# Optimization experiments

Hardware: AMD Instinct MI355X
Metric: run time of the kernel (lower is better)

## Reference

```python
import jax, jax.numpy as jnp
import numpy as np

DIM = 2048
N_HEADS = 16
N_KV_HEADS = 4
HEAD_DIM = 128
SLIDING_WINDOW = 1024
ROPE_BASE = 10000.0


def _rotate_half(x):
    d = x.shape[-1] // 2
    return jnp.concatenate((-x[..., d:], x[..., :d]), axis=-1)


def _rope_cos_sin(T, dtype):
    inv_freq = 1.0 / (ROPE_BASE ** (jnp.arange(0, HEAD_DIM, 2, dtype=jnp.float32) / HEAD_DIM))
    t = jnp.arange(T, dtype=jnp.float32)
    freqs = jnp.outer(t, inv_freq)            # [T, HEAD_DIM//2]
    emb = jnp.concatenate((freqs, freqs), axis=-1)  # [T, HEAD_DIM]
    return jnp.cos(emb).astype(dtype), jnp.sin(emb).astype(dtype)


def setup_inputs() -> dict:
    key = jax.random.key(0)
    kx, kq, kk, kv, ko = jax.random.split(key, 5)
    s_in = 1.0 / np.sqrt(DIM)
    s_o = 1.0 / np.sqrt(N_HEADS * HEAD_DIM)
    return {
        "x": jax.random.normal(kx, (1, 4096, DIM), dtype=jnp.float32),
        "Wq": jax.random.normal(kq, (DIM, N_HEADS * HEAD_DIM), dtype=jnp.float32) * s_in,
        "Wk": jax.random.normal(kk, (DIM, N_KV_HEADS * HEAD_DIM), dtype=jnp.float32) * s_in,
        "Wv": jax.random.normal(kv, (DIM, N_KV_HEADS * HEAD_DIM), dtype=jnp.float32) * s_in,
        "Wo": jax.random.normal(ko, (N_HEADS * HEAD_DIM, DIM), dtype=jnp.float32) * s_o,
    }


def reference(x, Wq, Wk, Wv, Wo):
    B, T, C = x.shape
    # projections -> [B, H, T, D]
    q = (x @ Wq).reshape(B, T, N_HEADS, HEAD_DIM).transpose(0, 2, 1, 3)
    k = (x @ Wk).reshape(B, T, N_KV_HEADS, HEAD_DIM).transpose(0, 2, 1, 3)
    v = (x @ Wv).reshape(B, T, N_KV_HEADS, HEAD_DIM).transpose(0, 2, 1, 3)

    cos, sin = _rope_cos_sin(T, x.dtype)      # [T, D], broadcast over B, H
    q = q * cos + _rotate_half(q) * sin
    k = k * cos + _rotate_half(k) * sin

    # GQA: repeat kv heads (repeat_interleave over head axis)
    kv_rep = N_HEADS // N_KV_HEADS
    k = jnp.repeat(k, kv_rep, axis=1)
    v = jnp.repeat(v, kv_rep, axis=1)

    scale = 1.0 / np.sqrt(HEAD_DIM)
    att = jnp.einsum("bhqd,bhkd->bhqk", q, k) * scale  # [B, H, T, T]

    i = jnp.arange(T)[:, None]
    j = jnp.arange(T)[None, :]
    allowed = (j <= i) & ((i - j) < SLIDING_WINDOW)     # causal + sliding window
    att = jnp.where(allowed, att, -jnp.inf)
    att = jax.nn.softmax(att, axis=-1)

    y = jnp.einsum("bhqk,bhkd->bhqd", att, v)           # [B, H, T, D]
    y = y.transpose(0, 2, 1, 3).reshape(B, T, N_HEADS * HEAD_DIM)
    return y @ Wo
```

## Files before the change

kernel.cpp:

```cpp
#include <hip/hip_runtime.h>
#include <math.h>

typedef __bf16 bf16;
typedef __bf16 bf16x8 __attribute__((ext_vector_type(8)));
typedef __bf16 bf16x4 __attribute__((ext_vector_type(4)));
typedef float f32x4 __attribute__((ext_vector_type(4)));

__device__ __forceinline__ void ldg_lds16(const bf16* g, bf16* l) {
#if __has_builtin(__builtin_amdgcn_global_load_lds)
    __builtin_amdgcn_global_load_lds(
        (const __attribute__((address_space(1))) void*)g,
        (__attribute__((address_space(3))) void*)l, 16, 0, 0);
#else
    *(bf16x8*)l = *(const bf16x8*)g;
#endif
}

__global__ void cvt_x(const float* __restrict__ X, bf16* __restrict__ Xb, int total8)
{
    int idx = blockIdx.x * 256 + threadIdx.x;
    if (idx >= total8) return;
    const float* p = X + (size_t)idx * 8;
    f32x4 a = *reinterpret_cast<const f32x4*>(p);
    f32x4 b = *reinterpret_cast<const f32x4*>(p + 4);
    bf16x8 r;
    r[0] = (bf16)a[0]; r[1] = (bf16)a[1]; r[2] = (bf16)a[2]; r[3] = (bf16)a[3];
    r[4] = (bf16)b[0]; r[5] = (bf16)b[1]; r[6] = (bf16)b[2]; r[7] = (bf16)b[3];
    *reinterpret_cast<bf16x8*>(Xb + (size_t)idx * 8) = r;
}

__global__ void cvt_wt3(const float* __restrict__ Wq, const float* __restrict__ Wk,
                        const float* __restrict__ Wv, bf16* __restrict__ Wt)
{
    __shared__ float t[32][33];
    int bx = blockIdx.x;
    const float* W; int Ncols, nbase;
    if (bx < 64)      { W = Wq; Ncols = 2048; nbase = 0;    }
    else if (bx < 80) { W = Wk; Ncols = 512;  nbase = 2048; bx -= 64; }
    else              { W = Wv; Ncols = 512;  nbase = 2560; bx -= 80; }
    const int n0 = bx * 32, k0 = blockIdx.y * 32;
    const int x = threadIdx.x, y = threadIdx.y;
    #pragma unroll
    for (int i = 0; i < 4; ++i)
        t[y + 8 * i][x] = W[(size_t)(k0 + y + 8 * i) * Ncols + n0 + x];
    __syncthreads();
    #pragma unroll
    for (int i = 0; i < 4; ++i)
        Wt[(size_t)(nbase + n0 + y + 8 * i) * 2048 + k0 + x] = (bf16)t[x][y + 8 * i];
}

__global__ void cvt_wt(const float* __restrict__ W, bf16* __restrict__ Wt, int Ncols)
{
    __shared__ float t[32][33];
    const int n0 = blockIdx.x * 32, k0 = blockIdx.y * 32;
    const int x = threadIdx.x, y = threadIdx.y;
    #pragma unroll
    for (int i = 0; i < 4; ++i)
        t[y + 8 * i][x] = W[(size_t)(k0 + y + 8 * i) * Ncols + n0 + x];
    __syncthreads();
    #pragma unroll
    for (int i = 0; i < 4; ++i)
        Wt[(size_t)(n0 + y + 8 * i) * 2048 + k0 + x] = (bf16)t[x][y + 8 * i];
}

__global__ __launch_bounds__(512, 2) void gemm256_qkv(
    const bf16* __restrict__ A, const bf16* __restrict__ Bt,
    bf16* __restrict__ Qo, bf16* __restrict__ Ko, bf16* __restrict__ Vt,
    int K)
{
    __shared__ __align__(16) bf16 smem[2 * 28672];

    const int tid  = threadIdx.x;
    const int lane = tid & 63;
    const int wave = tid >> 6;
    const int quad = lane >> 4;
    const int l16  = lane & 15;
    const int wm   = wave >> 2;
    const int wn   = wave & 3;

    const int m0 = blockIdx.y * 256;
    const int n0 = blockIdx.x * 192;

    int offA[4], offB[3];
    #pragma unroll
    for (int p = 0; p < 4; ++p) {
        int u = p * 512 + tid;
        int row = u >> 3;
        int kc8 = (u & 7) ^ (row & 7);
        offA[p] = (m0 + row) * K + kc8 * 8;
    }
    #pragma unroll
    for (int p = 0; p < 3; ++p) {
        int u = p * 512 + tid;
        int row = u >> 3;
        int kc8 = (u & 7) ^ (row & 7);
        offB[p] = (n0 + row) * K + kc8 * 8;
    }
    const int dstoff = tid * 8;

    const int xv = (l16 & 7) << 4;
    const int c0 = ((quad * 16) ^ xv) >> 1;
    const int c1 = ((64 + quad * 16) ^ xv) >> 1;
    const int rA = (wm * 128 + l16) * 64;
    const int rB = (wn * 48 + l16) * 64;

    f32x4 acc[8][3] = {};
    const int NT = K >> 6;

    auto stage = [&](int tt, int bsel) {
        bf16* as = smem + bsel * 28672;
        bf16* bs = as + 16384;
        const int koff = tt * 64;
        #pragma unroll
        for (int p = 0; p < 4; ++p)
            ldg_lds16(A + offA[p] + koff, as + p * 4096 + dstoff);
        #pragma unroll
        for (int p = 0; p < 3; ++p)
            ldg_lds16(Bt + offB[p] + koff, bs + p * 4096 + dstoff);
    };

    stage(0, 0);
    stage(1, 1);
    asm volatile("s_waitcnt vmcnt(7)" ::: "memory");
    __builtin_amdgcn_sched_barrier(0);
    __builtin_amdgcn_s_barrier();
    __builtin_amdgcn_sched_barrier(0);

    for (int t = 0; t < NT; ++t) {
        const bf16* As = smem + (t & 1) * 28672;
        const bf16* Bs = As + 16384;

        bf16x8 a0[8], b0[3];
        #pragma unroll
        for (int i = 0; i < 8; ++i)
            a0[i] = *(const bf16x8*)(As + rA + i * 1024 + c0);
        #pragma unroll
        for (int i = 0; i < 3; ++i)
            b0[i] = *(const bf16x8*)(Bs + rB + i * 1024 + c0);

        #pragma unroll
        for (int mi = 0; mi < 8; ++mi)
            #pragma unroll
            for (int ni = 0; ni < 3; ++ni)
                acc[mi][ni] = __builtin_amdgcn_mfma_f32_16x16x32_bf16(
                    a0[mi], b0[ni], acc[mi][ni], 0, 0, 0);

        bf16x8 a1[8], b1[3];
        #pragma unroll
        for (int i = 0; i < 8; ++i)
            a1[i] = *(const bf16x8*)(As + rA + i * 1024 + c1);
        #pragma unroll
        for (int i = 0; i < 3; ++i)
            b1[i] = *(const bf16x8*)(Bs + rB + i * 1024 + c1);

        asm volatile("s_waitcnt lgkmcnt(0)" ::: "memory");
        __builtin_amdgcn_sched_barrier(0);
        __builtin_amdgcn_s_barrier();
        __builtin_amdgcn_sched_barrier(0);

        if (t + 2 < NT) stage(t + 2, t & 1);

        __builtin_amdgcn_s_setprio(1);
        #pragma unroll
        for (int mi = 0; mi < 8; ++mi)
            #pragma unroll
            for (int ni = 0; ni < 3; ++ni)
                acc[mi][ni] = __builtin_amdgcn_mfma_f32_16x16x32_bf16(
                    a1[mi], b1[ni], acc[mi][ni], 0, 0, 0);
        __builtin_amdgcn_s_setprio(0);

        if (t + 2 < NT) {
            asm volatile("s_waitcnt vmcnt(7)" ::: "memory");
            __builtin_amdgcn_sched_barrier(0);
            __builtin_amdgcn_s_barrier();
            __builtin_amdgcn_sched_barrier(0);
        } else if (t == NT - 2) {
            asm volatile("s_waitcnt vmcnt(0)" ::: "memory");
            __builtin_amdgcn_sched_barrier(0);
            __builtin_amdgcn_s_barrier();
            __builtin_amdgcn_sched_barrier(0);
        }
    }

    #pragma unroll
    for (int mi = 0; mi < 8; ++mi) {
        #pragma unroll
        for (int ni = 0; ni < 3; ++ni) {
            const int row = m0 + wm * 128 + mi * 16 + quad * 4;
            const int col = n0 + wn * 48 + ni * 16 + l16;
            const int cb  = n0 + wn * 48 + ni * 16;
            if (cb < 2048) {
                #pragma unroll
                for (int r = 0; r < 4; ++r)
                    Qo[(size_t)(row + r) * 2048 + col] = (bf16)acc[mi][ni][r];
            } else if (cb < 2560) {
                #pragma unroll
                for (int r = 0; r < 4; ++r)
                    Ko[(size_t)(row + r) * 512 + (col - 2048)] = (bf16)acc[mi][ni][r];
            } else {
                bf16x4 v;
                #pragma unroll
                for (int r = 0; r < 4; ++r) v[r] = (bf16)acc[mi][ni][r];
                *reinterpret_cast<bf16x4*>(&Vt[(size_t)(col - 2560) * 4096 + row]) = v;
            }
        }
    }
}

__global__ __launch_bounds__(512, 2) void gemm_out(
    const bf16* __restrict__ A, const bf16* __restrict__ Bt,
    float* __restrict__ C, int K)
{
    __shared__ __align__(16) bf16 smem[2 * 24576];

    const int tid  = threadIdx.x;
    const int lane = tid & 63;
    const int wave = tid >> 6;
    const int quad = lane >> 4;
    const int l16  = lane & 15;
    const int wm   = wave >> 1;
    const int wn   = wave & 1;

    const int m0 = blockIdx.y * 256;
    const int n0 = blockIdx.x * 128;

    int offA[4], offB[2];
    #pragma unroll
    for (int p = 0; p < 4; ++p) {
        int u = p * 512 + tid;
        int row = u >> 3;
        int kc8 = (u & 7) ^ (row & 7);
        offA[p] = (m0 + row) * K + kc8 * 8;
    }
    #pragma unroll
    for (int p = 0; p < 2; ++p) {
        int u = p * 512 + tid;
        int row = u >> 3;
        int kc8 = (u & 7) ^ (row & 7);
        offB[p] = (n0 + row) * K + kc8 * 8;
    }
    const int dstoff = tid * 8;

    const int xv = (l16 & 7) << 4;
    const int c0 = ((quad * 16) ^ xv) >> 1;
    const int c1 = ((64 + quad * 16) ^ xv) >> 1;
    const int rA = (wm * 64 + l16) * 64;
    const int rB = (wn * 64 + l16) * 64;

    f32x4 acc[4][4] = {};
    const int NT = K >> 6;

    auto stage = [&](int tt, int bsel) {
        bf16* as = smem + bsel * 24576;
        bf16* bs = as + 16384;
        const int koff = tt * 64;
        #pragma unroll
        for (int p = 0; p < 4; ++p)
            ldg_lds16(A + offA[p] + koff, as + p * 4096 + dstoff);
        #pragma unroll
        for (int p = 0; p < 2; ++p)
            ldg_lds16(Bt + offB[p] + koff, bs + p * 4096 + dstoff);
    };

    stage(0, 0);
    stage(1, 1);
    asm volatile("s_waitcnt vmcnt(6)" ::: "memory");
    __builtin_amdgcn_sched_barrier(0);
    __builtin_amdgcn_s_barrier();
    __builtin_amdgcn_sched_barrier(0);

    for (int t = 0; t < NT; ++t) {
        const bf16* As = smem + (t & 1) * 24576;
        const bf16* Bs = As + 16384;

        bf16x8 a0[4], b0[4];
        #pragma unroll
        for (int i = 0; i < 4; ++i)
            a0[i] = *(const bf16x8*)(As + rA + i * 1024 + c0);
        #pragma unroll
        for (int i = 0; i < 4; ++i)
            b0[i] = *(const bf16x8*)(Bs + rB + i * 1024 + c0);

        #pragma unroll
        for (int mi = 0; mi < 4; ++mi)
            #pragma unroll
            for (int ni = 0; ni < 4; ++ni)
                acc[mi][ni] = __builtin_amdgcn_mfma_f32_16x16x32_bf16(
                    a0[mi], b0[ni], acc[mi][ni], 0, 0, 0);

        bf16x8 a1[4], b1[4];
        #pragma unroll
        for (int i = 0; i < 4; ++i)
            a1[i] = *(const bf16x8*)(As + rA + i * 1024 + c1);
        #pragma unroll
        for (int i = 0; i < 4; ++i)
            b1[i] = *(const bf16x8*)(Bs + rB + i * 1024 + c1);

        asm volatile("s_waitcnt lgkmcnt(0)" ::: "memory");
        __builtin_amdgcn_sched_barrier(0);
        __builtin_amdgcn_s_barrier();
        __builtin_amdgcn_sched_barrier(0);

        if (t + 2 < NT) stage(t + 2, t & 1);

        __builtin_amdgcn_s_setprio(1);
        #pragma unroll
        for (int mi = 0; mi < 4; ++mi)
            #pragma unroll
            for (int ni = 0; ni < 4; ++ni)
                acc[mi][ni] = __builtin_amdgcn_mfma_f32_16x16x32_bf16(
                    a1[mi], b1[ni], acc[mi][ni], 0, 0, 0);
        __builtin_amdgcn_s_setprio(0);

        if (t + 2 < NT) {
            asm volatile("s_waitcnt vmcnt(6)" ::: "memory");
            __builtin_amdgcn_sched_barrier(0);
            __builtin_amdgcn_s_barrier();
            __builtin_amdgcn_sched_barrier(0);
        } else if (t == NT - 2) {
            asm volatile("s_waitcnt vmcnt(0)" ::: "memory");
            __builtin_amdgcn_sched_barrier(0);
            __builtin_amdgcn_s_barrier();
            __builtin_amdgcn_sched_barrier(0);
        }
    }

    #pragma unroll
    for (int mi = 0; mi < 4; ++mi) {
        #pragma unroll
        for (int ni = 0; ni < 4; ++ni) {
            const int row = m0 + wm * 64 + mi * 16 + quad * 4;
            const int col = n0 + wn * 64 + ni * 16 + l16;
            #pragma unroll
            for (int r = 0; r < 4; ++r)
                C[(size_t)(row + r) * 2048 + col] = acc[mi][ni][r];
        }
    }
}

__global__ void rope_k(bf16* __restrict__ Kb, int total)
{
    int idx = blockIdx.x * 256 + threadIdx.x;
    if (idx >= total) return;
    int j  = idx & 63;
    int th = idx >> 6;
    int t  = th >> 2;

    bf16* p = Kb + (size_t)th * 128;
    const float NEG_LN1E4_64 = -0.14391155806323211f;
    float inv_freq = expf(NEG_LN1E4_64 * (float)j);
    float ang = (float)t * inv_freq;
    float c = cosf(ang), s = sinf(ang);
    float q0 = (float)p[j], q1 = (float)p[j + 64];
    p[j]      = (bf16)(q0 * c - q1 * s);
    p[j + 64] = (bf16)(q1 * c + q0 * s);
}

__global__ __launch_bounds__(256) void attn_v10(
    const bf16* __restrict__ Q, const bf16* __restrict__ K,
    const bf16* __restrict__ Vt, bf16* __restrict__ Y)
{
    const float scale = 0.08838834764831845f;

    __shared__ __align__(16) bf16 Ks[2 * 64 * 128];
    __shared__ __align__(16) bf16 Vs[2 * 128 * 64];
    __shared__ __align__(16) bf16 Pl[4][16 * 72];

    const int tid  = threadIdx.x;
    const int lane = tid & 63;
    const int wave = tid >> 6;
    const int quad = lane >> 4;
    const int l16  = lane & 15;

    const int i0  = (gridDim.x - 1 - blockIdx.x) * 64;
    const int h   = blockIdx.y;
    const int kvh = h >> 2;
    const int q0  = i0 + wave * 16;
    bf16* Plw = Pl[wave];

    const int ks = (i0 >= 1024) ? (i0 - 1024) : 0;
    const int nsteps = (i0 + 64 - ks) >> 6;

    auto stage = [&](int tt, int bsel) {
        const int k0s = ks + tt * 64;
        bf16* kd = Ks + bsel * 8192;
        bf16* vd = Vs + bsel * 8192;
        #pragma unroll
        for (int p = 0; p < 4; ++p) {
            int u = p * 256 + tid;
            int kk = u >> 4, sc = u & 15;
            ldg_lds16(K + (size_t)(k0s + kk) * 512 + kvh * 128 + (sc ^ (kk & 15)) * 8,
                      kd + u * 8);
        }
        #pragma unroll
        for (int p = 0; p < 4; ++p) {
            int u = p * 256 + tid;
            int d = u >> 3, sc = u & 7;
            ldg_lds16(Vt + (size_t)(kvh * 128 + d) * 4096 + k0s + (sc ^ (d & 7)) * 8,
                      vd + u * 8);
        }
    };

    bf16x8 qr_[4];
    {
        const bf16* qp = Q + (size_t)(q0 + l16) * 2048 + h * 128 + quad * 8;
        #pragma unroll
        for (int c = 0; c < 4; ++c)
            qr_[c] = *reinterpret_cast<const bf16x8*>(qp + c * 32);
    }

    stage(0, 0);
    stage(1, 1);

    bf16x8 qf[4];
    {
        const float NEG_LN1E4_64 = -0.14391155806323211f;
        const float tf = (float)(q0 + l16);
        #pragma unroll
        for (int c = 0; c < 2; ++c) {
            #pragma unroll
            for (int i = 0; i < 8; ++i) {
                float inv_freq = expf(NEG_LN1E4_64 * (float)(c * 32 + quad * 8 + i));
                float ang = tf * inv_freq;
                float cs = cosf(ang), sn = sinf(ang);
                float a = (float)qr_[c][i], b = (float)qr_[c + 2][i];
                qf[c][i]     = (bf16)(a * cs - b * sn);
                qf[c + 2][i] = (bf16)(b * cs + a * sn);
            }
        }
    }

    f32x4 o[8] = {};
    float lsum[4] = {0.f, 0.f, 0.f, 0.f};

    asm volatile("s_waitcnt vmcnt(8)" ::: "memory");
    __builtin_amdgcn_sched_barrier(0);
    __builtin_amdgcn_s_barrier();
    __builtin_amdgcn_sched_barrier(0);

    for (int t = 0; t < nsteps; ++t) {
        const int b  = t & 1;
        const int k0 = ks + t * 64;
        const bf16* Kb = Ks + b * 8192;
        const bf16* Vb = Vs + b * 8192;

        f32x4 s[4];
        __builtin_amdgcn_s_setprio(1);
        #pragma unroll
        for (int kh = 0; kh < 4; ++kh) {
            const int kk = kh * 16 + l16;
            f32x4 sv = {};
            #pragma unroll
            for (int c = 0; c < 4; ++c) {
                bf16x8 kf = *reinterpret_cast<const bf16x8*>(
                    &Kb[kk * 128 + (((c * 4 + quad) ^ (kk & 15)) * 8)]);
                sv = __builtin_amdgcn_mfma_f32_16x16x32_bf16(qf[c], kf, sv, 0, 0, 0);
            }
            s[kh] = sv;
        }
        __builtin_amdgcn_s_setprio(0);

        #pragma unroll
        for (int kh = 0; kh < 4; ++kh) {
            const int key = k0 + kh * 16 + l16;
            #pragma unroll
            for (int r = 0; r < 4; ++r) {
                const int qrow = q0 + quad * 4 + r;
                bool ok = (unsigned)(qrow - key) < 1024u;
                float pv = ok ? __expf(s[kh][r] * scale) : 0.f;
                lsum[r] += pv;
                Plw[(quad * 4 + r) * 72 + kh * 16 + l16] = (bf16)pv;
            }
        }

        bf16x8 pf0 = *reinterpret_cast<const bf16x8*>(&Plw[l16 * 72 + quad * 8]);
        bf16x8 pf1 = *reinterpret_cast<const bf16x8*>(&Plw[l16 * 72 + 32 + quad * 8]);
        __builtin_amdgcn_s_setprio(1);
        #pragma unroll
        for (int n = 0; n < 8; ++n) {
            const int d = n * 16 + l16;
            bf16x8 v0 = *reinterpret_cast<const bf16x8*>(
                &Vb[d * 64 + (((quad) ^ (d & 7)) * 8)]);
            bf16x8 v1 = *reinterpret_cast<const bf16x8*>(
                &Vb[d * 64 + (((4 + quad) ^ (d & 7)) * 8)]);
            o[n] = __builtin_amdgcn_mfma_f32_16x16x32_bf16(pf0, v0, o[n], 0, 0, 0);
            o[n] = __builtin_amdgcn_mfma_f32_16x16x32_bf16(pf1, v1, o[n], 0, 0, 0);
        }
        __builtin_amdgcn_s_setprio(0);

        asm volatile("s_waitcnt lgkmcnt(0)" ::: "memory");
        __builtin_amdgcn_sched_barrier(0);
        __builtin_amdgcn_s_barrier();
        __builtin_amdgcn_sched_barrier(0);

        if (t + 2 < nsteps) {
            stage(t + 2, b);
            asm volatile("s_waitcnt vmcnt(8)" ::: "memory");
        } else {
            asm volatile("s_waitcnt vmcnt(0)" ::: "memory");
        }
        __builtin_amdgcn_sched_barrier(0);
        __builtin_amdgcn_s_barrier();
        __builtin_amdgcn_sched_barrier(0);
    }

    #pragma unroll
    for (int r = 0; r < 4; ++r) {
        #pragma unroll
        for (int off = 1; off < 16; off <<= 1)
            lsum[r] += __shfl_xor(lsum[r], off, 64);
    }
    #pragma unroll
    for (int r = 0; r < 4; ++r) {
        int row = q0 + quad * 4 + r;
        float inv = (lsum[r] > 0.f) ? 1.f / lsum[r] : 0.f;
        #pragma unroll
        for (int n = 0; n < 8; ++n)
            Y[(size_t)row * 2048 + h * 128 + n * 16 + l16] = (bf16)(o[n][r] * inv);
    }
}

extern "C" void kernel_launch(void* const* d_in, const int* in_sizes, int n_in,
                              void* d_out, int out_size, void* d_ws, size_t ws_size,
                              hipStream_t stream)
{
    const float* x  = (const float*)d_in[0];
    const float* Wq = (const float*)d_in[1];
    const float* Wk = (const float*)d_in[2];
    const float* Wv = (const float*)d_in[3];
    const float* Wo = (const float*)d_in[4];
    float* out = (float*)d_out;

    const int T = 4096, DIM = 2048;

    char* po = (char*)d_out;
    bf16* Qb = (bf16*)(po);
    bf16* Kb = (bf16*)(po + (16u << 20));
    bf16* Vtb = (bf16*)(po + (20u << 20));

    char* ws = (char*)d_ws;
    bf16* xb    = (bf16*)(ws);
    bf16* Wqkvt = (bf16*)(ws + (16u << 20));
    bf16* Yb    = (bf16*)(ws);
    bf16* Wot   = (bf16*)(ws + (16u << 20));

    cvt_x<<<dim3(T * DIM / 8 / 256), 256, 0, stream>>>(x, xb, T * DIM / 8);

    dim3 tb(32, 8);
    cvt_wt3<<<dim3(96, 64), tb, 0, stream>>>(Wq, Wk, Wv, Wqkvt);

    gemm256_qkv<<<dim3(3072 / 192, T / 256), 512, 0, stream>>>(
        xb, Wqkvt, Qb, Kb, Vtb, DIM);

    cvt_wt<<<dim3(2048 / 32, 64), tb, 0, stream>>>(Wo, Wot, 2048);

    int ktot = T * 4 * 64;
    rope_k<<<(ktot + 255) / 256, 256, 0, stream>>>(Kb, ktot);

    attn_v10<<<dim3(T / 64, 16), 256, 0, stream>>>(Qb, Kb, Vtb, Yb);

    gemm_out<<<dim3(2048 / 128, T / 256), 512, 0, stream>>>(
        Yb, Wot, out, DIM);
}
```

Baseline: 289.3 us.

## Precompute RoPE table, skip masking on full tiles, swizzle P scratch

```diff
diff --git a/kernel.cpp b/kernel.cpp
--- a/kernel.cpp
+++ b/kernel.cpp
@@ -14,6 +14,18 @@
 #else
     *(bf16x8*)l = *(const bf16x8*)g;
 #endif
+}
+
+__global__ void rope_cs(float2* __restrict__ CS, int total)
+{
+    int idx = blockIdx.x * 256 + threadIdx.x;
+    if (idx >= total) return;
+    int j = idx & 63;
+    int t = idx >> 6;
+    const float NEG_LN1E4_64 = -0.14391155806323211f;
+    float inv_freq = expf(NEG_LN1E4_64 * (float)j);
+    float ang = (float)t * inv_freq;
+    CS[idx] = make_float2(cosf(ang), sinf(ang));
 }
 
 __global__ void cvt_x(const float* __restrict__ X, bf16* __restrict__ Xb, int total8)
@@ -338,7 +350,8 @@
     }
 }
 
-__global__ void rope_k(bf16* __restrict__ Kb, int total)
+__global__ void rope_k(const float2* __restrict__ CS, bf16* __restrict__ Kb,
+                       int total)
 {
     int idx = blockIdx.x * 256 + threadIdx.x;
     if (idx >= total) return;
@@ -347,24 +360,22 @@
     int t  = th >> 2;
 
     bf16* p = Kb + (size_t)th * 128;
-    const float NEG_LN1E4_64 = -0.14391155806323211f;
-    float inv_freq = expf(NEG_LN1E4_64 * (float)j);
-    float ang = (float)t * inv_freq;
-    float c = cosf(ang), s = sinf(ang);
+    float2 cs = CS[t * 64 + j];
     float q0 = (float)p[j], q1 = (float)p[j + 64];
-    p[j]      = (bf16)(q0 * c - q1 * s);
-    p[j + 64] = (bf16)(q1 * c + q0 * s);
-}
-
-__global__ __launch_bounds__(256) void attn_v10(
+    p[j]      = (bf16)(q0 * cs.x - q1 * cs.y);
+    p[j + 64] = (bf16)(q1 * cs.x + q0 * cs.y);
+}
+
+__global__ __launch_bounds__(256) void attn_v11(
     const bf16* __restrict__ Q, const bf16* __restrict__ K,
-    const bf16* __restrict__ Vt, bf16* __restrict__ Y)
+    const bf16* __restrict__ Vt, bf16* __restrict__ Y,
+    const float2* __restrict__ CS)
 {
     const float scale = 0.08838834764831845f;
 
     __shared__ __align__(16) bf16 Ks[2 * 64 * 128];
     __shared__ __align__(16) bf16 Vs[2 * 128 * 64];
-    __shared__ __align__(16) bf16 Pl[4][16 * 72];
+    __shared__ __align__(16) bf16 Pl[4][16 * 64];
 
     const int tid  = threadIdx.x;
     const int lane = tid & 63;
@@ -402,31 +413,32 @@
     };
 
     bf16x8 qr_[4];
+    float2 csv[16];
     {
         const bf16* qp = Q + (size_t)(q0 + l16) * 2048 + h * 128 + quad * 8;
         #pragma unroll
         for (int c = 0; c < 4; ++c)
             qr_[c] = *reinterpret_cast<const bf16x8*>(qp + c * 32);
+        const float2* csp = CS + (size_t)(q0 + l16) * 64 + quad * 8;
+        #pragma unroll
+        for (int c = 0; c < 2; ++c)
+            #pragma unroll
+            for (int i = 0; i < 8; ++i)
+                csv[c * 8 + i] = csp[c * 32 + i];
     }
 
     stage(0, 0);
     stage(1, 1);
 
     bf16x8 qf[4];
-    {
-        const float NEG_LN1E4_64 = -0.14391155806323211f;
-        const float tf = (float)(q0 + l16);
-        #pragma unroll
-        for (int c = 0; c < 2; ++c) {
-            #pragma unroll
-            for (int i = 0; i < 8; ++i) {
-                float inv_freq = expf(NEG_LN1E4_64 * (float)(c * 32 + quad * 8 + i));
-                float ang = tf * inv_freq;
-                float cs = cosf(ang), sn = sinf(ang);
-                float a = (float)qr_[c][i], b = (float)qr_[c + 2][i];
-                qf[c][i]     = (bf16)(a * cs - b * sn);
-                qf[c + 2][i] = (bf16)(b * cs + a * sn);
-            }
+    #pragma unroll
+    for (int c = 0; c < 2; ++c) {
+        #pragma unroll
+        for (int i = 0; i < 8; ++i) {
+            float cs_ = csv[c * 8 + i].x, sn = csv[c * 8 + i].y;
+            float a = (float)qr_[c][i], b = (float)qr_[c + 2][i];
+            qf[c][i]     = (bf16)(a * cs_ - b * sn);
+            qf[c + 2][i] = (bf16)(b * cs_ + a * sn);
         }
     }
 
@@ -460,21 +472,42 @@
         }
         __builtin_amdgcn_s_setprio(0);
 
-        #pragma unroll
-        for (int kh = 0; kh < 4; ++kh) {
-            const int key = k0 + kh * 16 + l16;
-            #pragma unroll
-            for (int r = 0; r < 4; ++r) {
-                const int qrow = q0 + quad * 4 + r;
-                bool ok = (unsigned)(qrow - key) < 1024u;
-                float pv = ok ? __expf(s[kh][r] * scale) : 0.f;
-                lsum[r] += pv;
-                Plw[(quad * 4 + r) * 72 + kh * 16 + l16] = (bf16)pv;
+        const bool full = (k0 + 63 <= q0) && (q0 + 15 - k0 < 1024);
+        if (full) {
+            #pragma unroll
+            for (int kh = 0; kh < 4; ++kh) {
+                #pragma unroll
+                for (int r = 0; r < 4; ++r) {
+                    float pv = __expf(s[kh][r] * scale);
+                    lsum[r] += pv;
+                    const int row = quad * 4 + r;
+                    const int idx = row * 64 +
+                        ((((kh * 2 + (l16 >> 3)) ^ (row & 7)) << 3) | (l16 & 7));
+                    Plw[idx] = (bf16)pv;
+                }
             }
-        }
-
-        bf16x8 pf0 = *reinterpret_cast<const bf16x8*>(&Plw[l16 * 72 + quad * 8]);
-        bf16x8 pf1 = *reinterpret_cast<const bf16x8*>(&Plw[l16 * 72 + 32 + quad * 8]);
+        } else {
+            #pragma unroll
+            for (int kh = 0; kh < 4; ++kh) {
+                const int key = k0 + kh * 16 + l16;
+                #pragma unroll
+                for (int r = 0; r < 4; ++r) {
+                    const int qrow = q0 + quad * 4 + r;
+                    bool ok = (unsigned)(qrow - key) < 1024u;
+                    float pv = ok ? __expf(s[kh][r] * scale) : 0.f;
+                    lsum[r] += pv;
+                    const int row = quad * 4 + r;
+                    const int idx = row * 64 +
+                        ((((kh * 2 + (l16 >> 3)) ^ (row & 7)) << 3) | (l16 & 7));
+                    Plw[idx] = (bf16)pv;
+                }
+            }
+        }
+
+        bf16x8 pf0 = *reinterpret_cast<const bf16x8*>(
+            &Plw[l16 * 64 + ((quad ^ (l16 & 7)) << 3)]);
+        bf16x8 pf1 = *reinterpret_cast<const bf16x8*>(
+            &Plw[l16 * 64 + (((4 + quad) ^ (l16 & 7)) << 3)]);
         __builtin_amdgcn_s_setprio(1);
         #pragma unroll
         for (int n = 0; n < 8; ++n) {
@@ -534,9 +567,10 @@
     const int T = 4096, DIM = 2048;
 
     char* po = (char*)d_out;
-    bf16* Qb = (bf16*)(po);
-    bf16* Kb = (bf16*)(po + (16u << 20));
+    bf16* Qb  = (bf16*)(po);
+    bf16* Kb  = (bf16*)(po + (16u << 20));
     bf16* Vtb = (bf16*)(po + (20u << 20));
+    float2* CS = (float2*)(po + (24u << 20));
 
     char* ws = (char*)d_ws;
     bf16* xb    = (bf16*)(ws);
@@ -544,6 +578,8 @@
     bf16* Yb    = (bf16*)(ws);
     bf16* Wot   = (bf16*)(ws + (16u << 20));
 
+    rope_cs<<<dim3(T * 64 / 256), 256, 0, stream>>>(CS, T * 64);
+
     cvt_x<<<dim3(T * DIM / 8 / 256), 256, 0, stream>>>(x, xb, T * DIM / 8);
 
     dim3 tb(32, 8);
@@ -555,9 +591,9 @@
     cvt_wt<<<dim3(2048 / 32, 64), tb, 0, stream>>>(Wo, Wot, 2048);
 
     int ktot = T * 4 * 64;
-    rope_k<<<(ktot + 255) / 256, 256, 0, stream>>>(Kb, ktot);
-
-    attn_v10<<<dim3(T / 64, 16), 256, 0, stream>>>(Qb, Kb, Vtb, Yb);
+    rope_k<<<(ktot + 255) / 256, 256, 0, stream>>>(CS, Kb, ktot);
+
+    attn_v11<<<dim3(T / 64, 16), 256, 0, stream>>>(Qb, Kb, Vtb, Yb, CS);
 
     gemm_out<<<dim3(2048 / 128, T / 256), 512, 0, stream>>>(
         Yb, Wot, out, DIM);
```

Measured after the change: 278.7 us. 3.7% less time.
